# Kernel tuning notes

Measured on AMD Instinct MI355X. Metric: run time of the kernel, lower is better.

The kernel has to match this reference:

```python
import jax, jax.numpy as jnp
import numpy as np

N = 1_000_000   # nodes (== number of edges, required by the original code)
E = 1_000_000
NODE_IN, NODE_OUT = 64, 64
EDGE_IN, EDGE_OUT = 16, 64
GRAPH_IN, GRAPH_OUT = 32, 64
ALPHA = 0.2


def setup_inputs() -> dict:
    key = jax.random.key(0)
    ks = jax.random.split(key, 10)
    seg_ids = jnp.sort(jax.random.randint(ks[0], (E,), 0, N, dtype=jnp.int32))
    node_fts = jax.random.normal(ks[1], (N, NODE_IN), dtype=jnp.float32)
    edge_fts = jax.random.normal(ks[2], (E, EDGE_IN), dtype=jnp.float32)
    graph_fts = jax.random.normal(ks[3], (1, GRAPH_IN), dtype=jnp.float32)
    # `edges` is a float matrix whose first column holds the segment ids
    edges = jax.random.normal(ks[4], (E, EDGE_IN), dtype=jnp.float32)
    edges = edges.at[:, 0].set(seg_ids.astype(jnp.float32))
    # parameters (xavier-ish scaled normals)
    def xavier(k, shape, gain=1.0):
        fan_in, fan_out = shape[0], shape[1]
        std = gain * np.sqrt(2.0 / (fan_in + fan_out))
        return jax.random.normal(k, shape, dtype=jnp.float32) * std
    W_node = xavier(ks[5], (NODE_IN, NODE_OUT))
    W_edge = xavier(ks[6], (EDGE_IN, EDGE_OUT))
    W_graph = xavier(ks[7], (GRAPH_IN, GRAPH_OUT))
    a_node = xavier(ks[8], (NODE_OUT + GRAPH_OUT, 1), gain=1.414)
    a_edge = xavier(ks[9], (EDGE_OUT + GRAPH_OUT, 1), gain=1.414)
    return {"node_fts": node_fts, "edge_fts": edge_fts, "graph_fts": graph_fts,
            "edges": edges, "seg_ids": seg_ids, "W_node": W_node,
            "W_edge": W_edge, "W_graph": W_graph, "a_node": a_node,
            "a_edge": a_edge}


def _segment_softmax(att, seg_ids, num_segments):
    # exp(clamp(att)) normalized by per-segment sums, gathered back per row
    att = jnp.exp(jnp.clip(att, -2.0, 2.0))
    sums = jax.ops.segment_sum(att, seg_ids, num_segments=num_segments)
    return att / sums[seg_ids]


def reference(node_fts, edge_fts, graph_fts, edges, seg_ids,
              W_node, W_edge, W_graph, a_node, a_edge):
    h_v = node_fts @ W_node                      # [N, NODE_OUT]
    e_v = edges @ W_edge                         # [E, EDGE_OUT]
    g_v = graph_fts @ W_graph                    # [1, GRAPH_OUT]
    G = g_v.shape[1]
    # concat([g_v.repeat, h_v]) @ a == g_v @ a[:G] + h_v @ a[G:]  (no big concat)
    node_att = jax.nn.leaky_relu(
        (g_v @ a_node[:G] + h_v @ a_node[G:]).squeeze(-1), ALPHA)   # [N]
    edge_att = jax.nn.leaky_relu(
        (g_v @ a_edge[:G] + e_v @ a_edge[G:]).squeeze(-1), ALPHA)   # [E]
    n = node_fts.shape[0]
    node_attention_norm = _segment_softmax(node_att, seg_ids, n)
    edge_attention_norm = _segment_softmax(edge_att, seg_ids, n)
    return (node_attention_norm, edge_attention_norm)
```

## Files before the change

### kernel.cpp

```cpp
#include <hip/hip_runtime.h>

#define ALPHA 0.2f

__global__ void ga_consts_kernel(const float* __restrict__ graph_fts,
                                 const float* __restrict__ W_node,
                                 const float* __restrict__ W_edge,
                                 const float* __restrict__ W_graph,
                                 const float* __restrict__ a_node,
                                 const float* __restrict__ a_edge,
                                 float* __restrict__ consts) {
    const int k = threadIdx.x;

    float g = 0.f;
    #pragma unroll
    for (int c = 0; c < 32; ++c) g += graph_fts[c] * W_graph[c * 64 + k];

    float wn = 0.f;
    #pragma unroll
    for (int c = 0; c < 64; ++c) wn += W_node[k * 64 + c] * a_node[64 + c];
    consts[k] = wn;

    if (k < 16) {
        float we = 0.f;
        #pragma unroll
        for (int c = 0; c < 64; ++c) we += W_edge[k * 64 + c] * a_edge[64 + c];
        consts[64 + k] = we;
    }

    float cn = g * a_node[k];
    float ce = g * a_edge[k];
    #pragma unroll
    for (int off = 32; off > 0; off >>= 1) {
        cn += __shfl_down(cn, off);
        ce += __shfl_down(ce, off);
    }
    if (k == 0) { consts[80] = cn; consts[81] = ce; }
}

__global__ void ga_node_att_kernel(const float* __restrict__ node_fts,
                                   const int* __restrict__ seg_ids,
                                   const float* __restrict__ consts,
                                   float* __restrict__ out_e,
                                   float* __restrict__ sums_node,
                                   int N) {
    const int lane16 = threadIdx.x & 15;
    const int gid = blockIdx.x * blockDim.x + threadIdx.x;
    const int group = gid >> 4;
    const int ngroups = (gridDim.x * blockDim.x) >> 4;

    const float4 w = *reinterpret_cast<const float4*>(&consts[lane16 * 4]);
    const float c_node = consts[80];

    for (int row = group; row < N; row += ngroups) {
        const float4 x = *reinterpret_cast<const float4*>(
            &node_fts[(size_t)row * 64 + lane16 * 4]);
        float d = x.x * w.x + x.y * w.y + x.z * w.z + x.w * w.w;
        d += __shfl_xor(d, 1);
        d += __shfl_xor(d, 2);
        d += __shfl_xor(d, 4);
        d += __shfl_xor(d, 8);
        if (lane16 == 0) {
            float att = c_node + d;
            att = att > 0.f ? att : ALPHA * att;
            att = fminf(fmaxf(att, -2.f), 2.f);
            const float e = expf(att);
            out_e[row] = e;
            atomicAdd(&sums_node[seg_ids[row]], e);
        }
    }
}

__global__ void ga_edge_att_kernel(const float* __restrict__ edges,
                                   const int* __restrict__ seg_ids,
                                   const float* __restrict__ consts,
                                   float* __restrict__ out_e,
                                   float* __restrict__ sums_edge,
                                   int E) {
    const int lane4 = threadIdx.x & 3;
    const int gid = blockIdx.x * blockDim.x + threadIdx.x;
    const int group = gid >> 2;
    const int ngroups = (gridDim.x * blockDim.x) >> 2;

    const float4 w = *reinterpret_cast<const float4*>(&consts[64 + lane4 * 4]);
    const float c_edge = consts[81];

    for (int row = group; row < E; row += ngroups) {
        const float4 x = *reinterpret_cast<const float4*>(
            &edges[(size_t)row * 16 + lane4 * 4]);
        float d = x.x * w.x + x.y * w.y + x.z * w.z + x.w * w.w;
        d += __shfl_xor(d, 1);
        d += __shfl_xor(d, 2);
        if (lane4 == 0) {
            float att = c_edge + d;
            att = att > 0.f ? att : ALPHA * att;
            att = fminf(fmaxf(att, -2.f), 2.f);
            const float e = expf(att);
            out_e[row] = e;
            atomicAdd(&sums_edge[seg_ids[row]], e);
        }
    }
}

__global__ void ga_norm_kernel(const int* __restrict__ seg_ids,
                               const float* __restrict__ sums_node,
                               const float* __restrict__ sums_edge,
                               float* __restrict__ out, int N) {
    int j = blockIdx.x * blockDim.x + threadIdx.x;
    const int stride = gridDim.x * blockDim.x;
    for (; j < N; j += stride) {
        const int s = seg_ids[j];
        out[j]     = out[j]     / sums_node[s];
        out[N + j] = out[N + j] / sums_edge[s];
    }
}

extern "C" void kernel_launch(void* const* d_in, const int* in_sizes, int n_in,
                              void* d_out, int out_size, void* d_ws, size_t ws_size,
                              hipStream_t stream) {
    const float* node_fts  = (const float*)d_in[0];
    const float* graph_fts = (const float*)d_in[2];
    const float* edges     = (const float*)d_in[3];
    const int*   seg_ids   = (const int*)  d_in[4];
    const float* W_node    = (const float*)d_in[5];
    const float* W_edge    = (const float*)d_in[6];
    const float* W_graph   = (const float*)d_in[7];
    const float* a_node    = (const float*)d_in[8];
    const float* a_edge    = (const float*)d_in[9];

    const int N = in_sizes[0] / 64;
    const int E = in_sizes[4];

    float* out       = (float*)d_out;
    float* sums_node = (float*)d_ws;
    float* sums_edge = sums_node + N;
    float* consts    = sums_edge + N;

    hipMemsetAsync(d_ws, 0, (size_t)(2 * N) * sizeof(float), stream);

    ga_consts_kernel<<<1, 64, 0, stream>>>(graph_fts, W_node, W_edge, W_graph,
                                           a_node, a_edge, consts);
    ga_node_att_kernel<<<2048, 256, 0, stream>>>(node_fts, seg_ids, consts,
                                                 out, sums_node, N);
    ga_edge_att_kernel<<<1024, 256, 0, stream>>>(edges, seg_ids, consts,
                                                 out + N, sums_edge, E);
    ga_norm_kernel<<<2048, 256, 0, stream>>>(seg_ids, sums_node, sums_edge, out, N);
}
```

Baseline: 441.7 us.

## Fuse consts, node and edge attention into one kernel; vectorize normalization

Merges the constant-computation kernel, the node-attention kernel and the edge-attention kernel into a single launch. Each block recomputes the small folded weight vectors into shared memory, then block ranges are split between node rows and edge rows. This removes two launches and the serialization between node and edge passes, letting both streams of memory traffic overlap. The normalization kernel is vectorized to float4/int4 accesses with fewer blocks. The cost is that every block redundantly reads the weight matrices to rebuild the constants.

```diff
diff --git a/kernel.cpp b/kernel.cpp
--- a/kernel.cpp
+++ b/kernel.cpp
@@ -1,116 +1,128 @@
 #include <hip/hip_runtime.h>
 
 #define ALPHA 0.2f
+#define NODE_BLOCKS 2048
+#define EDGE_BLOCKS 512
 
-__global__ void ga_consts_kernel(const float* __restrict__ graph_fts,
-                                 const float* __restrict__ W_node,
-                                 const float* __restrict__ W_edge,
-                                 const float* __restrict__ W_graph,
-                                 const float* __restrict__ a_node,
-                                 const float* __restrict__ a_edge,
-                                 float* __restrict__ consts) {
-    const int k = threadIdx.x;
+__global__ __launch_bounds__(256)
+void ga_att_fused(const float* __restrict__ node_fts,
+                  const float* __restrict__ edges,
+                  const float* __restrict__ graph_fts,
+                  const int* __restrict__ seg_ids,
+                  const float* __restrict__ W_node,
+                  const float* __restrict__ W_edge,
+                  const float* __restrict__ W_graph,
+                  const float* __restrict__ a_node,
+                  const float* __restrict__ a_edge,
+                  float* __restrict__ out,
+                  float* __restrict__ sums_node,
+                  float* __restrict__ sums_edge,
+                  int N, int E) {
+    __shared__ __align__(16) float cst[84];
+    const int t = threadIdx.x;
 
-    float g = 0.f;
-    #pragma unroll
-    for (int c = 0; c < 32; ++c) g += graph_fts[c] * W_graph[c * 64 + k];
+    if (t < 64) {
+        float g = 0.f;
+        #pragma unroll
+        for (int c = 0; c < 32; ++c) g += graph_fts[c] * W_graph[c * 64 + t];
 
-    float wn = 0.f;
-    #pragma unroll
-    for (int c = 0; c < 64; ++c) wn += W_node[k * 64 + c] * a_node[64 + c];
-    consts[k] = wn;
+        float wn = 0.f;
+        #pragma unroll
+        for (int c = 0; c < 64; ++c) wn += W_node[t * 64 + c] * a_node[64 + c];
+        cst[t] = wn;
 
-    if (k < 16) {
-        float we = 0.f;
+        if (t < 16) {
+            float we = 0.f;
+            #pragma unroll
+            for (int c = 0; c < 64; ++c) we += W_edge[t * 64 + c] * a_edge[64 + c];
+            cst[64 + t] = we;
+        }
+        float cn = g * a_node[t];
+        float ce = g * a_edge[t];
         #pragma unroll
-        for (int c = 0; c < 64; ++c) we += W_edge[k * 64 + c] * a_edge[64 + c];
-        consts[64 + k] = we;
+        for (int off = 32; off > 0; off >>= 1) {
+            cn += __shfl_down(cn, off);
+            ce += __shfl_down(ce, off);
+        }
+        if (t == 0) { cst[80] = cn; cst[81] = ce; }
     }
+    __syncthreads();
 
-    float cn = g * a_node[k];
-    float ce = g * a_edge[k];
-    #pragma unroll
-    for (int off = 32; off > 0; off >>= 1) {
-        cn += __shfl_down(cn, off);
-        ce += __shfl_down(ce, off);
-    }
-    if (k == 0) { consts[80] = cn; consts[81] = ce; }
-}
-
-__global__ void ga_node_att_kernel(const float* __restrict__ node_fts,
-                                   const int* __restrict__ seg_ids,
-                                   const float* __restrict__ consts,
-                                   float* __restrict__ out_e,
-                                   float* __restrict__ sums_node,
-                                   int N) {
-    const int lane16 = threadIdx.x & 15;
-    const int gid = blockIdx.x * blockDim.x + threadIdx.x;
-    const int group = gid >> 4;
-    const int ngroups = (gridDim.x * blockDim.x) >> 4;
-
-    const float4 w = *reinterpret_cast<const float4*>(&consts[lane16 * 4]);
-    const float c_node = consts[80];
-
-    for (int row = group; row < N; row += ngroups) {
-        const float4 x = *reinterpret_cast<const float4*>(
-            &node_fts[(size_t)row * 64 + lane16 * 4]);
-        float d = x.x * w.x + x.y * w.y + x.z * w.z + x.w * w.w;
-        d += __shfl_xor(d, 1);
-        d += __shfl_xor(d, 2);
-        d += __shfl_xor(d, 4);
-        d += __shfl_xor(d, 8);
-        if (lane16 == 0) {
-            float att = c_node + d;
-            att = att > 0.f ? att : ALPHA * att;
-            att = fminf(fmaxf(att, -2.f), 2.f);
-            const float e = expf(att);
-            out_e[row] = e;
-            atomicAdd(&sums_node[seg_ids[row]], e);
+    if (blockIdx.x < NODE_BLOCKS) {
+        const int lane16 = t & 15;
+        const float4 w = *reinterpret_cast<const float4*>(&cst[lane16 * 4]);
+        const float c_node = cst[80];
+        const int group = ((blockIdx.x << 8) + t) >> 4;
+        const int ngroups = (NODE_BLOCKS << 8) >> 4;
+        for (int row = group; row < N; row += ngroups) {
+            const float4 x = *reinterpret_cast<const float4*>(
+                &node_fts[(size_t)row * 64 + lane16 * 4]);
+            float d = x.x * w.x + x.y * w.y + x.z * w.z + x.w * w.w;
+            d += __shfl_xor(d, 1);
+            d += __shfl_xor(d, 2);
+            d += __shfl_xor(d, 4);
+            d += __shfl_xor(d, 8);
+            if (lane16 == 0) {
+                float att = c_node + d;
+                att = att > 0.f ? att : ALPHA * att;
+                att = fminf(fmaxf(att, -2.f), 2.f);
+                const float e = expf(att);
+                out[row] = e;
+                atomicAdd(&sums_node[seg_ids[row]], e);
+            }
+        }
+    } else {
+        const int lane4 = t & 3;
+        const float4 w = *reinterpret_cast<const float4*>(&cst[64 + lane4 * 4]);
+        const float c_edge = cst[81];
+        const int bid = blockIdx.x - NODE_BLOCKS;
+        const int group = ((bid << 8) + t) >> 2;
+        const int ngroups = (EDGE_BLOCKS << 8) >> 2;
+        for (int row = group; row < E; row += ngroups) {
+            const float4 x = *reinterpret_cast<const float4*>(
+                &edges[(size_t)row * 16 + lane4 * 4]);
+            float d = x.x * w.x + x.y * w.y + x.z * w.z + x.w * w.w;
+            d += __shfl_xor(d, 1);
+            d += __shfl_xor(d, 2);
+            if (lane4 == 0) {
+                float att = c_edge + d;
+                att = att > 0.f ? att : ALPHA * att;
+                att = fminf(fmaxf(att, -2.f), 2.f);
+                const float e = expf(att);
+                out[N + row] = e;
+                atomicAdd(&sums_edge[seg_ids[row]], e);
+            }
         }
     }
 }
 
-__global__ void ga_edge_att_kernel(const float* __restrict__ edges,
-                                   const int* __restrict__ seg_ids,
-                                   const float* __restrict__ consts,
-                                   float* __restrict__ out_e,
-                                   float* __restrict__ sums_edge,
-                                   int E) {
-    const int lane4 = threadIdx.x & 3;
-    const int gid = blockIdx.x * blockDim.x + threadIdx.x;
-    const int group = gid >> 2;
-    const int ngroups = (gridDim.x * blockDim.x) >> 2;
-
-    const float4 w = *reinterpret_cast<const float4*>(&consts[64 + lane4 * 4]);
-    const float c_edge = consts[81];
-
-    for (int row = group; row < E; row += ngroups) {
-        const float4 x = *reinterpret_cast<const float4*>(
-            &edges[(size_t)row * 16 + lane4 * 4]);
-        float d = x.x * w.x + x.y * w.y + x.z * w.z + x.w * w.w;
-        d += __shfl_xor(d, 1);
-        d += __shfl_xor(d, 2);
-        if (lane4 == 0) {
-            float att = c_edge + d;
-            att = att > 0.f ? att : ALPHA * att;
-            att = fminf(fmaxf(att, -2.f), 2.f);
-            const float e = expf(att);
-            out_e[row] = e;
-            atomicAdd(&sums_edge[seg_ids[row]], e);
+__global__ __launch_bounds__(256)
+void ga_norm_kernel(const int* __restrict__ seg_ids,
+                    const float* __restrict__ sums_node,
+                    const float* __restrict__ sums_edge,
+                    float* __restrict__ out, int N) {
+    const int idx = blockIdx.x * blockDim.x + threadIdx.x;
+    const int stride = gridDim.x * blockDim.x;
+    if ((N & 3) == 0) {
+        const int n4 = N >> 2;
+        float* out2 = out + N;
+        for (int q = idx; q < n4; q += stride) {
+            const int4 s = reinterpret_cast<const int4*>(seg_ids)[q];
+            float4 o1 = reinterpret_cast<float4*>(out)[q];
+            float4 o2 = reinterpret_cast<float4*>(out2)[q];
+            o1.x /= sums_node[s.x]; o1.y /= sums_node[s.y];
+            o1.z /= sums_node[s.z]; o1.w /= sums_node[s.w];
+            o2.x /= sums_edge[s.x]; o2.y /= sums_edge[s.y];
+            o2.z /= sums_edge[s.z]; o2.w /= sums_edge[s.w];
+            reinterpret_cast<float4*>(out)[q] = o1;
+            reinterpret_cast<float4*>(out2)[q] = o2;
         }
-    }
-}
-
-__global__ void ga_norm_kernel(const int* __restrict__ seg_ids,
-                               const float* __restrict__ sums_node,
-                               const float* __restrict__ sums_edge,
-                               float* __restrict__ out, int N) {
-    int j = blockIdx.x * blockDim.x + threadIdx.x;
-    const int stride = gridDim.x * blockDim.x;
-    for (; j < N; j += stride) {
-        const int s = seg_ids[j];
-        out[j]     = out[j]     / sums_node[s];
-        out[N + j] = out[N + j] / sums_edge[s];
+    } else {
+        for (int j = idx; j < N; j += stride) {
+            const int s = seg_ids[j];
+            out[j]     /= sums_node[s];
+            out[N + j] /= sums_edge[s];
+        }
     }
 }
 
@@ -133,15 +145,13 @@
     float* out       = (float*)d_out;
     float* sums_node = (float*)d_ws;
     float* sums_edge = sums_node + N;
-    float* consts    = sums_edge + N;
 
     hipMemsetAsync(d_ws, 0, (size_t)(2 * N) * sizeof(float), stream);
 
-    ga_consts_kernel<<<1, 64, 0, stream>>>(graph_fts, W_node, W_edge, W_graph,
-                                           a_node, a_edge, consts);
-    ga_node_att_kernel<<<2048, 256, 0, stream>>>(node_fts, seg_ids, consts,
-                                                 out, sums_node, N);
-    ga_edge_att_kernel<<<1024, 256, 0, stream>>>(edges, seg_ids, consts,
-                                                 out + N, sums_edge, E);
-    ga_norm_kernel<<<2048, 256, 0, stream>>>(seg_ids, sums_node, sums_edge, out, N);
+    ga_att_fused<<<NODE_BLOCKS + EDGE_BLOCKS, 256, 0, stream>>>(
+        node_fts, edges, graph_fts, seg_ids, W_node, W_edge, W_graph,
+        a_node, a_edge, out, sums_node, sums_edge, N, E);
+
+    ga_norm_kernel<<<1024, 256, 0, stream>>>(seg_ids, sums_node, sums_edge,
+                                             out, N);
 }
```

New measurement: 468.1 us. 1.06x slower.
